# Kernel optimization log

Measured on AMD Instinct MI355X. Metric: run time of the kernel, lower is better.

The kernel has to match this reference:

```python
import jax, jax.numpy as jnp
import numpy as np

DIM = 768
NUM_HEADS = 12
HEAD_DIM = DIM // NUM_HEADS
GRID = 32  # H == W
EPS = 1e-6


def setup_inputs() -> dict:
    key = jax.random.key(0)
    ks = jax.random.split(key, 8)
    B, N = 8, GRID * GRID
    x = jax.random.normal(ks[0], (B, N, DIM), dtype=jnp.float32)
    policy = jax.random.randint(ks[1], (B, N, 1), 0, 2).astype(jnp.float32)
    qkv_w = jax.random.normal(ks[2], (3 * DIM, DIM), dtype=jnp.float32) * 0.02
    qkv_b = jax.random.normal(ks[3], (3 * DIM,), dtype=jnp.float32) * 0.02
    proj_w = jax.random.normal(ks[4], (DIM, DIM), dtype=jnp.float32) * 0.02
    proj_b = jax.random.normal(ks[5], (DIM,), dtype=jnp.float32) * 0.02
    rel_pos_h = jax.random.normal(ks[6], (2 * GRID - 1, HEAD_DIM), dtype=jnp.float32) * 0.02
    rel_pos_w = jax.random.normal(ks[7], (2 * GRID - 1, HEAD_DIM), dtype=jnp.float32) * 0.02
    return {"x": x, "policy": policy, "qkv_w": qkv_w, "qkv_b": qkv_b,
            "proj_w": proj_w, "proj_b": proj_b,
            "rel_pos_h": rel_pos_h, "rel_pos_w": rel_pos_w, "H": GRID, "W": GRID}


def _attention(x, policy, qkv_w, qkv_b, proj_w, proj_b, rel_pos_h, rel_pos_w, H, W):
    B, N, C = x.shape
    nh, hd = NUM_HEADS, C // NUM_HEADS
    scale = hd ** (-0.5)
    # qkv projection: [B,N,3C] -> [3, B*nh, N, hd]
    qkv = (x @ qkv_w.T + qkv_b).reshape(B, N, 3, nh, hd)
    qkv = qkv.transpose(2, 0, 3, 1, 4).reshape(3, B * nh, N, hd)
    q, k, v = qkv[0], qkv[1], qkv[2]
    attn = jnp.einsum("bqd,bkd->bqk", q * scale, k)  # [B*nh, N, N]
    # decomposed relative position bias (q_size == k_size == (H, W))
    coords = jnp.arange(H)
    Rh = rel_pos_h[coords[:, None] - coords[None, :] + (H - 1)]  # [H,H,hd]
    coords_w = jnp.arange(W)
    Rw = rel_pos_w[coords_w[:, None] - coords_w[None, :] + (W - 1)]  # [W,W,hd]
    r_q = q.reshape(B * nh, H, W, hd)
    rel_h = jnp.einsum("bhwc,hkc->bhwk", r_q, Rh)  # [B*nh,H,W,H]
    rel_w = jnp.einsum("bhwc,wkc->bhwk", r_q, Rw)  # [B*nh,H,W,W]
    attn = (attn.reshape(B * nh, H, W, H, W)
            + rel_h[:, :, :, :, None]
            + rel_w[:, :, :, None, :]).reshape(B * nh, N, N)
    # policy-masked softmax
    attn = attn.reshape(B, nh, N, N)
    ap = policy.reshape(B, 1, 1, N)
    ap = ap + (1.0 - ap) * jnp.eye(N, dtype=ap.dtype)  # always attend to self
    max_att = jnp.max(attn, axis=-1, keepdims=True)
    e = jnp.exp(attn - max_att).astype(jnp.float32) * ap.astype(jnp.float32)
    attn = ((e + EPS / N) / (jnp.sum(e, axis=-1, keepdims=True) + EPS)).astype(x.dtype)
    out = jnp.einsum("bqk,bkd->bqd", attn.reshape(B * nh, N, N), v)
    out = out.reshape(B, nh, N, hd).transpose(0, 2, 1, 3).reshape(B, N, C)
    return out @ proj_w.T + proj_b


def reference(x, policy, qkv_w, qkv_b, proj_w, proj_b, rel_pos_h, rel_pos_w, H, W):
    return _attention(x, policy, qkv_w, qkv_b, proj_w, proj_b, rel_pos_h, rel_pos_w, H, W)
```

## Files before the change

kernel.cpp:

```cpp
#include <hip/hip_runtime.h>
#include <hip/hip_bf16.h>

#define B_   8
#define N_   1024
#define C_   768
#define NH_  12
#define HD_  64
#define BH_  96
#define EPS_ 1e-6f
#define EPSN_ (1e-6f / 1024.0f)
#define SQ_  0.1803368801111244f
#define MNEG_ (-3.0e38f)

typedef __bf16 bf16;
typedef __attribute__((ext_vector_type(8))) __bf16  bf16x8;
typedef __attribute__((ext_vector_type(4))) __bf16  bf16x4;
typedef __attribute__((ext_vector_type(4))) float   floatx4;

#define MFMA16(a, b, c) __builtin_amdgcn_mfma_f32_16x16x32_bf16((a), (b), (c), 0, 0, 0)

__device__ __forceinline__ void gld16(const void* g, void* l) {
  typedef unsigned int u32;
  __builtin_amdgcn_global_load_lds(
      (const __attribute__((address_space(1))) u32*)g,
      (__attribute__((address_space(3))) u32*)l, 16, 0, 0);
}
__device__ __forceinline__ float bfu2f(unsigned int u) {
  union { unsigned int i; float f; } v; v.i = u << 16; return v.f;
}
__device__ __forceinline__ float bfhi2f(unsigned int u) {
  union { unsigned int i; float f; } v; v.i = u & 0xffff0000u; return v.f;
}
__device__ __forceinline__ unsigned short f2bfu(float f) {
  union { float f; unsigned int i; } v; v.f = f;
  return (unsigned short)((v.i + 0x7FFFu + ((v.i >> 16) & 1u)) >> 16);
}

__global__ __launch_bounds__(256) void prep_kernel(
    const float* __restrict__ x, const float* __restrict__ qkv_w,
    const float* __restrict__ proj_w, const float* __restrict__ relh,
    const float* __restrict__ relw,
    bf16* __restrict__ Xb, bf16* __restrict__ Wq, bf16* __restrict__ Wp,
    bf16* __restrict__ Rhb, bf16* __restrict__ Rwb) {
  int bid = blockIdx.x;
  if (bid < 8448) {
    const float* in; bf16* out; int i;
    if (bid < 6144)      { in = x;      out = Xb; i = bid * 256 + threadIdx.x; }
    else if (bid < 7872) { in = qkv_w;  out = Wq; i = (bid - 6144) * 256 + threadIdx.x; }
    else                 { in = proj_w; out = Wp; i = (bid - 7872) * 256 + threadIdx.x; }
    float4 v = ((const float4*)in)[i];
    bf16x4 o = {(bf16)v.x, (bf16)v.y, (bf16)v.z, (bf16)v.w};
    ((bf16x4*)out)[i] = o;
  } else {
    const float* in = (bid < 8464) ? relh : relw;
    bf16* out = (bid < 8464) ? Rhb : Rwb;
    int i = ((bid < 8464) ? (bid - 8448) : (bid - 8464)) * 256 + threadIdx.x;
    int r = i >> 6;
    out[i] = (r < 63) ? (bf16)(in[i] * 8.0f) : (bf16)0.0f;
  }
}

__global__ __launch_bounds__(256) void gemm_qkv(
    const bf16* __restrict__ X, const bf16* __restrict__ W,
    const float* __restrict__ bias,
    bf16* __restrict__ Qb, bf16* __restrict__ Kb, bf16* __restrict__ Vb) {
  __shared__ __align__(16) bf16 As[2][8192];
  __shared__ __align__(16) bf16 Bs[2][8192];
  const int tid = threadIdx.x;
  const int lane = tid & 63, quad = lane >> 4, c16 = lane & 15;
  const int wid = tid >> 6;
  const int wm = (wid >> 1) * 64, wn = (wid & 1) * 64;
  const int m0 = blockIdx.x * 128, n0 = blockIdx.y * 128;
  const bool flip = (blockIdx.y < 12);
  floatx4 acc[4][4];
#pragma unroll
  for (int i = 0; i < 4; ++i)
#pragma unroll
    for (int j = 0; j < 4; ++j) acc[i][j] = {0.f, 0.f, 0.f, 0.f};

  auto stage = [&](int k0, int buf) {
#pragma unroll
    for (int t = 0; t < 4; ++t) {
      int task = t * 256 + tid;
      int r = task >> 3, lg = (task & 7) ^ (r & 7);
      int wbase = (t * 256 + (tid & 192)) * 8;
      gld16(X + (size_t)(m0 + r) * 768 + k0 + lg * 8, &As[buf][wbase]);
      gld16(W + (size_t)(n0 + r) * 768 + k0 + lg * 8, &Bs[buf][wbase]);
    }
  };

  stage(0, 0);
  for (int it = 0; it < 12; ++it) {
    const int cur = it & 1;
    __syncthreads();
    if (it < 11) stage((it + 1) * 64, cur ^ 1);
#pragma unroll
    for (int kw = 0; kw < 2; ++kw) {
      bf16x8 af[4], bfr[4];
#pragma unroll
      for (int i = 0; i < 4; ++i) {
        int r = wm + i * 16 + c16, pg = (kw * 4 + quad) ^ (c16 & 7);
        af[i] = *(bf16x8*)&As[cur][r * 64 + pg * 8];
      }
#pragma unroll
      for (int j = 0; j < 4; ++j) {
        int r = wn + j * 16 + c16, pg = (kw * 4 + quad) ^ (c16 & 7);
        bfr[j] = *(bf16x8*)&Bs[cur][r * 64 + pg * 8];
      }
      if (flip) {
#pragma unroll
        for (int a = 0; a < 4; ++a)
#pragma unroll
          for (int b = 0; b < 4; ++b) acc[a][b] = MFMA16(bfr[a], af[b], acc[a][b]);
      } else {
#pragma unroll
        for (int i = 0; i < 4; ++i)
#pragma unroll
          for (int j = 0; j < 4; ++j) acc[i][j] = MFMA16(af[i], bfr[j], acc[i][j]);
      }
    }
  }
  if (flip) {
    const bool isQ = (blockIdx.y < 6);
    bf16* base = isQ ? Qb : Kb;
    const int off = isQ ? 0 : 768;
#pragma unroll
    for (int a = 0; a < 4; ++a) {
      int jb = n0 + wn + a * 16 + quad * 4;
      float4 b4 = *(const float4*)&bias[jb];
      int head = (jb - off) >> 6;
      int d = jb & 63;
#pragma unroll
      for (int b = 0; b < 4; ++b) {
        int tok = m0 + wm + b * 16 + c16;
        int bb = tok >> 10, n = tok & 1023;
        float v0 = acc[a][b][0] + b4.x, v1 = acc[a][b][1] + b4.y;
        float v2 = acc[a][b][2] + b4.z, v3 = acc[a][b][3] + b4.w;
        if (isQ) { v0 *= SQ_; v1 *= SQ_; v2 *= SQ_; v3 *= SQ_; }
        bf16x4 o = {(bf16)v0, (bf16)v1, (bf16)v2, (bf16)v3};
        *(bf16x4*)&base[(((size_t)bb * NH_ + head) * N_ + n) * HD_ + d] = o;
      }
    }
  } else {
#pragma unroll
    for (int jt = 0; jt < 4; ++jt) {
      int j = n0 + wn + jt * 16 + c16;
      float bj = bias[j];
      int rem = j - 1536, head = rem >> 6, d = rem & 63;
#pragma unroll
      for (int it = 0; it < 4; ++it) {
        int mbase = m0 + wm + it * 16 + quad * 4;
        int bb = mbase >> 10, n = mbase & 1023;
        bf16x4 o = {(bf16)(acc[it][jt][0] + bj), (bf16)(acc[it][jt][1] + bj),
                    (bf16)(acc[it][jt][2] + bj), (bf16)(acc[it][jt][3] + bj)};
        *(bf16x4*)&Vb[(((size_t)bb * NH_ + head) * HD_ + d) * N_ + n] = o;
      }
    }
  }
}

__global__ __launch_bounds__(256) void vsum_kernel(const bf16* __restrict__ Vb,
                                                   float* __restrict__ Vsum) {
  const int bh = blockIdx.x;
  const int d = threadIdx.x >> 2, part = threadIdx.x & 3;
  const bf16* Vg = Vb + (size_t)bh * (N_ * HD_) + d * N_ + part * 256;
  float s = 0.f;
  for (int i = 0; i < 32; ++i) {
    bf16x8 v = *(const bf16x8*)(Vg + i * 8);
#pragma unroll
    for (int e = 0; e < 8; ++e) s += (float)v[e];
  }
  __shared__ float red[64][4];
  red[d][part] = s;
  __syncthreads();
  if (part == 0) Vsum[bh * 64 + d] = red[d][0] + red[d][1] + red[d][2] + red[d][3];
}

__global__ __launch_bounds__(256, 3) void attn_mfma(
    const bf16* __restrict__ Qb, const bf16* __restrict__ Kb,
    const bf16* __restrict__ Vb, const float* __restrict__ policy,
    const bf16* __restrict__ Rh, const bf16* __restrict__ Rw,
    const float* __restrict__ Vsum, bf16* __restrict__ AO) {
  const int bh = blockIdx.x, qt = blockIdx.y;
  const int b = bh / NH_, head = bh % NH_;
  __shared__ __align__(16) bf16 Qs[4096];
  __shared__ __align__(16) bf16 Ks[2][4096];
  __shared__ __align__(16) bf16 Vt[2][4096];
  __shared__ unsigned short RHb[64][34];
  __shared__ unsigned short RWb[64][34];
  __shared__ __align__(16) float polf[1024];
  const int tid = threadIdx.x;
  const int wid = tid >> 6, lane = tid & 63, quad = lane >> 4, c16 = lane & 15;
  const int sw = c16 & 7;
  bf16* Ptw = Qs + wid * 1024;
  const floatx4 zero4 = {0.f, 0.f, 0.f, 0.f};

  const bf16* Qg = Qb + ((size_t)bh * N_ + qt * 64) * HD_;
  const bf16* Kg = Kb + (size_t)bh * (N_ * HD_);
  const bf16* Vg = Vb + (size_t)bh * (N_ * HD_);

  auto stageKV = [&](int kt2, int buf) {
#pragma unroll
    for (int t = 0; t < 2; ++t) {
      int task = t * 256 + tid;
      int r = task >> 3, lg = (task & 7) ^ (r & 7);
      int wbase = (t * 256 + (tid & 192)) * 8;
      gld16(Kg + (size_t)(kt2 * 64 + r) * 64 + lg * 8, &Ks[buf][wbase]);
      gld16(Vg + (size_t)r * N_ + kt2 * 64 + lg * 8, &Vt[buf][wbase]);
    }
  };

#pragma unroll
  for (int t = 0; t < 2; ++t) {
    int task = t * 256 + tid;
    int r = task >> 3, lg = (task & 7) ^ (r & 7);
    int wbase = (t * 256 + (tid & 192)) * 8;
    gld16(Qg + r * 64 + lg * 8, &Qs[wbase]);
    gld16(Rh + r * 64 + lg * 8, &Ks[0][wbase]);
  }
  gld16(policy + (size_t)b * N_ + tid * 4, &polf[(tid & 192) * 4]);
  __syncthreads();

  stageKV(0, 1);

  {
    float4 p4 = *(float4*)&polf[tid * 4];
    float4 m4 = make_float4((p4.x != 0.f) ? 0.f : MNEG_, (p4.y != 0.f) ? 0.f : MNEG_,
                            (p4.z != 0.f) ? 0.f : MNEG_, (p4.w != 0.f) ? 0.f : MNEG_);
    *(float4*)&polf[tid * 4] = m4;
  }

  bf16x8 aq0 = *(bf16x8*)&Qs[(wid * 16 + c16) * 64 + (quad ^ sw) * 8];
  bf16x8 aq1 = *(bf16x8*)&Qs[(wid * 16 + c16) * 64 + ((4 + quad) ^ sw) * 8];

  {
    floatx4 racc[4];
#pragma unroll
    for (int nt = 0; nt < 4; ++nt) {
      int r = nt * 16 + c16;
      bf16x8 b0 = *(bf16x8*)&Ks[0][r * 64 + (quad ^ sw) * 8];
      bf16x8 b1 = *(bf16x8*)&Ks[0][r * 64 + ((4 + quad) ^ sw) * 8];
      racc[nt] = MFMA16(aq1, b1, MFMA16(aq0, b0, zero4));
    }
#pragma unroll
    for (int nt = 0; nt < 4; ++nt)
#pragma unroll
      for (int reg = 0; reg < 4; ++reg) {
        int rloc = wid * 16 + quad * 4 + reg;
        int hh = 2 * qt + (rloc >> 5);
        int krow = hh + 31 - (nt * 16 + c16);
        if ((unsigned)krow < 32u) RHb[rloc][krow] = f2bfu(racc[nt][reg]);
      }
  }
  __syncthreads();
#pragma unroll
  for (int t = 0; t < 2; ++t) {
    int task = t * 256 + tid;
    int r = task >> 3, lg = (task & 7) ^ (r & 7);
    gld16(Rw + r * 64 + lg * 8, &Ks[0][(t * 256 + (tid & 192)) * 8]);
  }
  __syncthreads();
  {
    floatx4 racc[4];
#pragma unroll
    for (int nt = 0; nt < 4; ++nt) {
      int r = nt * 16 + c16;
      bf16x8 b0 = *(bf16x8*)&Ks[0][r * 64 + (quad ^ sw) * 8];
      bf16x8 b1 = *(bf16x8*)&Ks[0][r * 64 + ((4 + quad) ^ sw) * 8];
      racc[nt] = MFMA16(aq1, b1, MFMA16(aq0, b0, zero4));
    }
#pragma unroll
    for (int nt = 0; nt < 4; ++nt)
#pragma unroll
      for (int reg = 0; reg < 4; ++reg) {
        int rloc = wid * 16 + quad * 4 + reg;
        int kcol = (rloc & 31) + 31 - (nt * 16 + c16);
        if ((unsigned)kcol < 32u) RWb[rloc][kcol] = f2bfu(racc[nt][reg]);
      }
  }

  float rwv0[4], rwv1[4];
#pragma unroll
  for (int reg = 0; reg < 4; ++reg) {
    int rloc = wid * 16 + quad * 4 + reg;
    rwv0[reg] = bfu2f(RWb[rloc][c16]);
    rwv1[reg] = bfu2f(RWb[rloc][16 + c16]);
  }
  int ptoff[4][4];
#pragma unroll
  for (int reg = 0; reg < 4; ++reg) {
    int prow = quad * 4 + reg;
#pragma unroll
    for (int nt = 0; nt < 4; ++nt)
      ptoff[reg][nt] = prow * 64 + (c16 & 7) +
                       (((nt * 2 + (c16 >> 3)) ^ (prow & 7)) << 3);
  }

  float l_part[4] = {0.f, 0.f, 0.f, 0.f};
  floatx4 o_acc[4];
#pragma unroll
  for (int i = 0; i < 4; ++i) o_acc[i] = zero4;
  int nqr[4];
#pragma unroll
  for (int reg = 0; reg < 4; ++reg) nqr[reg] = qt * 64 + wid * 16 + quad * 4 + reg;

  for (int kt = 0; kt < 16; ++kt) {
    const int cur = (kt + 1) & 1;
    __syncthreads();
    if (kt < 15) stageKV(kt + 1, kt & 1);

    floatx4 init[4];
    float mv0 = polf[kt * 64 + c16],      mv1 = polf[kt * 64 + 16 + c16];
    float mv2 = polf[kt * 64 + 32 + c16], mv3 = polf[kt * 64 + 48 + c16];
#pragma unroll
    for (int reg = 0; reg < 4; ++reg) {
      int rloc = wid * 16 + quad * 4 + reg;
      unsigned int rhp = *(const unsigned int*)&RHb[rloc][kt * 2];
      float rh0 = bfu2f(rhp & 0xffffu), rh1 = bfhi2f(rhp);
      float m0 = mv0, m1 = mv1, m2 = mv2, m3 = mv3;
      if (kt == qt && c16 == quad * 4 + reg) {
        if (wid == 0) m0 = 0.f;
        else if (wid == 1) m1 = 0.f;
        else if (wid == 2) m2 = 0.f;
        else m3 = 0.f;
      }
      init[0][reg] = rh0 + rwv0[reg] + m0;
      init[1][reg] = rh0 + rwv1[reg] + m1;
      init[2][reg] = rh1 + rwv0[reg] + m2;
      init[3][reg] = rh1 + rwv1[reg] + m3;
    }

    floatx4 s[4];
#pragma unroll
    for (int nt = 0; nt < 4; ++nt) {
      int r = nt * 16 + c16;
      bf16x8 bk0 = *(bf16x8*)&Ks[cur][r * 64 + (quad ^ sw) * 8];
      bf16x8 bk1 = *(bf16x8*)&Ks[cur][r * 64 + ((4 + quad) ^ sw) * 8];
      s[nt] = MFMA16(aq1, bk1, MFMA16(aq0, bk0, init[nt]));
    }

#pragma unroll
    for (int reg = 0; reg < 4; ++reg) {
#pragma unroll
      for (int nt = 0; nt < 4; ++nt) {
        float e = exp2f(s[nt][reg]);
        l_part[reg] += e;
        Ptw[ptoff[reg][nt]] = (bf16)e;
      }
    }

#pragma unroll
    for (int kw2 = 0; kw2 < 2; ++kw2) {
      bf16x8 ap = *(bf16x8*)&Ptw[c16 * 64 + ((kw2 * 4 + quad) ^ sw) * 8];
#pragma unroll
      for (int dt = 0; dt < 4; ++dt) {
        int r = dt * 16 + c16;
        bf16x8 bv = *(bf16x8*)&Vt[cur][r * 64 + ((kw2 * 4 + quad) ^ sw) * 8];
        o_acc[dt] = MFMA16(ap, bv, o_acc[dt]);
      }
    }
  }

  float inv[4];
#pragma unroll
  for (int reg = 0; reg < 4; ++reg) {
    float l = l_part[reg];
#pragma unroll
    for (int d = 1; d < 16; d <<= 1) l += __shfl_xor(l, d, 64);
    inv[reg] = 1.f / (l + EPS_);
  }
#pragma unroll
  for (int dt = 0; dt < 4; ++dt) {
    int d = dt * 16 + c16;
    float vs = Vsum[bh * 64 + d];
#pragma unroll
    for (int reg = 0; reg < 4; ++reg) {
      float o = (o_acc[dt][reg] + EPSN_ * vs) * inv[reg];
      AO[((size_t)b * N_ + nqr[reg]) * C_ + head * HD_ + d] = (bf16)o;
    }
  }
}

__global__ __launch_bounds__(256) void gemm_proj(
    const bf16* __restrict__ A, const bf16* __restrict__ W,
    const float* __restrict__ bias, float* __restrict__ Out) {
  __shared__ __align__(16) bf16 As[2][8192];
  __shared__ __align__(16) bf16 Bs[2][8192];
  const int tid = threadIdx.x;
  const int lane = tid & 63, quad = lane >> 4, c16 = lane & 15;
  const int wid = tid >> 6;
  const int wm = (wid >> 1) * 64, wn = (wid & 1) * 64;
  const int m0 = blockIdx.x * 128, n0 = blockIdx.y * 128;
  floatx4 acc[4][4];
#pragma unroll
  for (int i = 0; i < 4; ++i)
#pragma unroll
    for (int j = 0; j < 4; ++j) acc[i][j] = {0.f, 0.f, 0.f, 0.f};

  auto stage = [&](int k0, int buf) {
#pragma unroll
    for (int t = 0; t < 4; ++t) {
      int task = t * 256 + tid;
      int r = task >> 3, lg = (task & 7) ^ (r & 7);
      int wbase = (t * 256 + (tid & 192)) * 8;
      gld16(A + (size_t)(m0 + r) * 768 + k0 + lg * 8, &As[buf][wbase]);
      gld16(W + (size_t)(n0 + r) * 768 + k0 + lg * 8, &Bs[buf][wbase]);
    }
  };

  stage(0, 0);
  for (int it = 0; it < 12; ++it) {
    const int cur = it & 1;
    __syncthreads();
    if (it < 11) stage((it + 1) * 64, cur ^ 1);
#pragma unroll
    for (int kw = 0; kw < 2; ++kw) {
      bf16x8 af[4], bfr[4];
#pragma unroll
      for (int i = 0; i < 4; ++i) {
        int r = wm + i * 16 + c16, pg = (kw * 4 + quad) ^ (c16 & 7);
        af[i] = *(bf16x8*)&As[cur][r * 64 + pg * 8];
      }
#pragma unroll
      for (int j = 0; j < 4; ++j) {
        int r = wn + j * 16 + c16, pg = (kw * 4 + quad) ^ (c16 & 7);
        bfr[j] = *(bf16x8*)&Bs[cur][r * 64 + pg * 8];
      }
#pragma unroll
      for (int a = 0; a < 4; ++a)
#pragma unroll
        for (int b = 0; b < 4; ++b) acc[a][b] = MFMA16(bfr[a], af[b], acc[a][b]);
    }
  }
#pragma unroll
  for (int a = 0; a < 4; ++a) {
    int jb = n0 + wn + a * 16 + quad * 4;
    float4 b4 = *(const float4*)&bias[jb];
#pragma unroll
    for (int b = 0; b < 4; ++b) {
      int m = m0 + wm + b * 16 + c16;
      float4 o = make_float4(acc[a][b][0] + b4.x, acc[a][b][1] + b4.y,
                             acc[a][b][2] + b4.z, acc[a][b][3] + b4.w);
      *(float4*)&Out[(size_t)m * 768 + jb] = o;
    }
  }
}

extern "C" void kernel_launch(void* const* d_in, const int* in_sizes, int n_in,
                              void* d_out, int out_size, void* d_ws, size_t ws_size,
                              hipStream_t stream) {
  const float* x      = (const float*)d_in[0];
  const float* policy = (const float*)d_in[1];
  const float* qkv_w  = (const float*)d_in[2];
  const float* qkv_b  = (const float*)d_in[3];
  const float* proj_w = (const float*)d_in[4];
  const float* proj_b = (const float*)d_in[5];
  const float* relh   = (const float*)d_in[6];
  const float* relw   = (const float*)d_in[7];

  char* ws = (char*)d_ws;
  bf16* Xbf   = (bf16*)(ws);
  bf16* Wqkv  = (bf16*)(ws + 12582912);
  bf16* Wproj = (bf16*)(ws + 16121856);
  bf16* Rhb   = (bf16*)(ws + 17301504);
  bf16* Rwb   = (bf16*)(ws + 17309696);
  bf16* Qb    = (bf16*)(ws + 17317888);
  bf16* Kb    = (bf16*)(ws + 29900800);
  bf16* Vb    = (bf16*)(ws + 42483712);
  bf16* AOb   = (bf16*)(ws + 55066624);
  float* Vsum = (float*)(ws + 67649536);

  prep_kernel<<<8480, 256, 0, stream>>>(x, qkv_w, proj_w, relh, relw,
                                        Xbf, Wqkv, Wproj, Rhb, Rwb);
  gemm_qkv<<<dim3(64, 18), 256, 0, stream>>>(Xbf, Wqkv, qkv_b, Qb, Kb, Vb);
  vsum_kernel<<<BH_, 256, 0, stream>>>(Vb, Vsum);
  attn_mfma<<<dim3(BH_, 16), 256, 0, stream>>>(Qb, Kb, Vb, policy, Rhb, Rwb,
                                               Vsum, AOb);
  gemm_proj<<<dim3(64, 6), 256, 0, stream>>>(AOb, Wproj, proj_b, (float*)d_out);
}
```

Baseline: 230.3 us.

## Keep attention probabilities in registers via transposed S and permuted K rows

The attention kernel now computes S transposed (K as the A operand, Q as B), and the K rows are loaded into shared memory in a permuted order so that the exp'd probabilities, once packed into bf16 pairs, line up directly as the A operand of the PV MFMA. This drops the per-tile LDS round trip for P and the Q staging buffer. The policy mask is now built as per-lane bitmasks through ballots instead of a float array in shared memory. Rh/Rw are read straight from global memory, several __syncthreads are removed, and launch bounds are raised to 4 blocks per CU. Risks are extra register pressure from the bitmasks and register-held P under the tighter occupancy bound, plus correctness of the intricate permutation.

```diff
diff --git a/kernel.cpp b/kernel.cpp
--- a/kernel.cpp
+++ b/kernel.cpp
@@ -176,23 +176,21 @@
   if (part == 0) Vsum[bh * 64 + d] = red[d][0] + red[d][1] + red[d][2] + red[d][3];
 }
 
-__global__ __launch_bounds__(256, 3) void attn_mfma(
+__global__ __launch_bounds__(256, 4) void attn_mfma(
     const bf16* __restrict__ Qb, const bf16* __restrict__ Kb,
     const bf16* __restrict__ Vb, const float* __restrict__ policy,
     const bf16* __restrict__ Rh, const bf16* __restrict__ Rw,
     const float* __restrict__ Vsum, bf16* __restrict__ AO) {
   const int bh = blockIdx.x, qt = blockIdx.y;
   const int b = bh / NH_, head = bh % NH_;
-  __shared__ __align__(16) bf16 Qs[4096];
   __shared__ __align__(16) bf16 Ks[2][4096];
   __shared__ __align__(16) bf16 Vt[2][4096];
-  __shared__ unsigned short RHb[64][34];
-  __shared__ unsigned short RWb[64][34];
-  __shared__ __align__(16) float polf[1024];
+  __shared__ unsigned int   RHb[64 * 16];
+  __shared__ unsigned short RWb[64 * 32];
   const int tid = threadIdx.x;
   const int wid = tid >> 6, lane = tid & 63, quad = lane >> 4, c16 = lane & 15;
   const int sw = c16 & 7;
-  bf16* Ptw = Qs + wid * 1024;
+  const int qloc = wid * 16 + c16;
   const floatx4 zero4 = {0.f, 0.f, 0.f, 0.f};
 
   const bf16* Qg = Qb + ((size_t)bh * N_ + qt * 64) * HD_;
@@ -203,44 +201,41 @@
 #pragma unroll
     for (int t = 0; t < 2; ++t) {
       int task = t * 256 + tid;
-      int r = task >> 3, lg = (task & 7) ^ (r & 7);
+      int p = task >> 3, g = task & 7;
+      int Tk = 32 * (p >> 5) + 4 * ((p >> 4) & 1) + 8 * ((p >> 2) & 3) + (p & 3);
       int wbase = (t * 256 + (tid & 192)) * 8;
-      gld16(Kg + (size_t)(kt2 * 64 + r) * 64 + lg * 8, &Ks[buf][wbase]);
-      gld16(Vg + (size_t)r * N_ + kt2 * 64 + lg * 8, &Vt[buf][wbase]);
+      gld16(Kg + (size_t)(kt2 * 64 + Tk) * 64 + ((g ^ (p & 7)) * 8), &Ks[buf][wbase]);
+      gld16(Vg + (size_t)p * N_ + kt2 * 64 + ((g ^ (p & 7)) * 8), &Vt[buf][wbase]);
     }
   };
 
-#pragma unroll
-  for (int t = 0; t < 2; ++t) {
-    int task = t * 256 + tid;
-    int r = task >> 3, lg = (task & 7) ^ (r & 7);
-    int wbase = (t * 256 + (tid & 192)) * 8;
-    gld16(Qg + r * 64 + lg * 8, &Qs[wbase]);
-    gld16(Rh + r * 64 + lg * 8, &Ks[0][wbase]);
-  }
-  gld16(policy + (size_t)b * N_ + tid * 4, &polf[(tid & 192) * 4]);
-  __syncthreads();
-
   stageKV(0, 1);
 
+  unsigned long long p64[4] = {0ull, 0ull, 0ull, 0ull};
   {
-    float4 p4 = *(float4*)&polf[tid * 4];
-    float4 m4 = make_float4((p4.x != 0.f) ? 0.f : MNEG_, (p4.y != 0.f) ? 0.f : MNEG_,
-                            (p4.z != 0.f) ? 0.f : MNEG_, (p4.w != 0.f) ? 0.f : MNEG_);
-    *(float4*)&polf[tid * 4] = m4;
-  }
-
-  bf16x8 aq0 = *(bf16x8*)&Qs[(wid * 16 + c16) * 64 + (quad ^ sw) * 8];
-  bf16x8 aq1 = *(bf16x8*)&Qs[(wid * 16 + c16) * 64 + ((4 + quad) ^ sw) * 8];
+    const float* Pg = policy + (size_t)b * N_;
+#pragma unroll
+    for (int kt = 0; kt < 16; ++kt) {
+      unsigned long long bal = __ballot(Pg[kt * 64 + lane] != 0.0f);
+      unsigned int w16 = (((unsigned int)bal >> (8 * quad)) & 0xFFu)
+                       | ((((unsigned int)(bal >> 32) >> (8 * quad)) & 0xFFu) << 8);
+      if (kt == qt && quad == ((qloc >> 3) & 3))
+        w16 |= 1u << (((qloc >> 5) << 3) | (qloc & 7));
+      p64[kt >> 2] |= (unsigned long long)w16 << (16 * (kt & 3));
+    }
+  }
+
+  bf16x8 qf0 = *(const bf16x8*)(Qg + qloc * 64 + quad * 8);
+  bf16x8 qf1 = *(const bf16x8*)(Qg + qloc * 64 + 32 + quad * 8);
 
   {
     floatx4 racc[4];
 #pragma unroll
     for (int nt = 0; nt < 4; ++nt) {
       int r = nt * 16 + c16;
-      bf16x8 b0 = *(bf16x8*)&Ks[0][r * 64 + (quad ^ sw) * 8];
-      bf16x8 b1 = *(bf16x8*)&Ks[0][r * 64 + ((4 + quad) ^ sw) * 8];
-      racc[nt] = MFMA16(aq1, b1, MFMA16(aq0, b0, zero4));
+      bf16x8 b0 = *(const bf16x8*)(Rh + r * 64 + quad * 8);
+      bf16x8 b1 = *(const bf16x8*)(Rh + r * 64 + 32 + quad * 8);
+      racc[nt] = MFMA16(qf1, b1, MFMA16(qf0, b0, zero4));
     }
 #pragma unroll
     for (int nt = 0; nt < 4; ++nt)
@@ -249,25 +244,18 @@
         int rloc = wid * 16 + quad * 4 + reg;
         int hh = 2 * qt + (rloc >> 5);
         int krow = hh + 31 - (nt * 16 + c16);
-        if ((unsigned)krow < 32u) RHb[rloc][krow] = f2bfu(racc[nt][reg]);
-      }
-  }
-  __syncthreads();
-#pragma unroll
-  for (int t = 0; t < 2; ++t) {
-    int task = t * 256 + tid;
-    int r = task >> 3, lg = (task & 7) ^ (r & 7);
-    gld16(Rw + r * 64 + lg * 8, &Ks[0][(t * 256 + (tid & 192)) * 8]);
-  }
-  __syncthreads();
+        if ((unsigned)krow < 32u)
+          ((unsigned short*)RHb)[rloc * 32 + krow] = f2bfu(racc[nt][reg]);
+      }
+  }
   {
     floatx4 racc[4];
 #pragma unroll
     for (int nt = 0; nt < 4; ++nt) {
       int r = nt * 16 + c16;
-      bf16x8 b0 = *(bf16x8*)&Ks[0][r * 64 + (quad ^ sw) * 8];
-      bf16x8 b1 = *(bf16x8*)&Ks[0][r * 64 + ((4 + quad) ^ sw) * 8];
-      racc[nt] = MFMA16(aq1, b1, MFMA16(aq0, b0, zero4));
+      bf16x8 b0 = *(const bf16x8*)(Rw + r * 64 + quad * 8);
+      bf16x8 b1 = *(const bf16x8*)(Rw + r * 64 + 32 + quad * 8);
+      racc[nt] = MFMA16(qf1, b1, MFMA16(qf0, b0, zero4));
     }
 #pragma unroll
     for (int nt = 0; nt < 4; ++nt)
@@ -275,108 +263,96 @@
       for (int reg = 0; reg < 4; ++reg) {
         int rloc = wid * 16 + quad * 4 + reg;
         int kcol = (rloc & 31) + 31 - (nt * 16 + c16);
-        if ((unsigned)kcol < 32u) RWb[rloc][kcol] = f2bfu(racc[nt][reg]);
-      }
-  }
-
-  float rwv0[4], rwv1[4];
-#pragma unroll
-  for (int reg = 0; reg < 4; ++reg) {
-    int rloc = wid * 16 + quad * 4 + reg;
-    rwv0[reg] = bfu2f(RWb[rloc][c16]);
-    rwv1[reg] = bfu2f(RWb[rloc][16 + c16]);
-  }
-  int ptoff[4][4];
-#pragma unroll
-  for (int reg = 0; reg < 4; ++reg) {
-    int prow = quad * 4 + reg;
-#pragma unroll
-    for (int nt = 0; nt < 4; ++nt)
-      ptoff[reg][nt] = prow * 64 + (c16 & 7) +
-                       (((nt * 2 + (c16 >> 3)) ^ (prow & 7)) << 3);
-  }
-
-  float l_part[4] = {0.f, 0.f, 0.f, 0.f};
+        if ((unsigned)kcol < 32u) RWb[rloc * 32 + kcol] = f2bfu(racc[nt][reg]);
+      }
+  }
+
+  float rwv[2][4];
+#pragma unroll
+  for (int p = 0; p < 2; ++p)
+#pragma unroll
+    for (int reg = 0; reg < 4; ++reg)
+      rwv[p][reg] = bfu2f(RWb[qloc * 32 + 8 * quad + 4 * p + reg]);
+
+  float l_lane = 0.f;
   floatx4 o_acc[4];
 #pragma unroll
   for (int i = 0; i < 4; ++i) o_acc[i] = zero4;
-  int nqr[4];
-#pragma unroll
-  for (int reg = 0; reg < 4; ++reg) nqr[reg] = qt * 64 + wid * 16 + quad * 4 + reg;
+
+  unsigned long long mm0 = p64[0], mm1 = p64[1], mm2 = p64[2], mm3 = p64[3];
 
   for (int kt = 0; kt < 16; ++kt) {
     const int cur = (kt + 1) & 1;
     __syncthreads();
     if (kt < 15) stageKV(kt + 1, kt & 1);
 
+    unsigned int w = (unsigned int)mm0 & 0xFFFFu;
+    mm0 = (mm0 >> 16) | (mm1 << 48);
+    mm1 = (mm1 >> 16) | (mm2 << 48);
+    mm2 = (mm2 >> 16) | (mm3 << 48);
+    mm3 >>= 16;
+    unsigned int rhp = RHb[qloc * 16 + kt];
+    float rh0 = bfu2f(rhp & 0xffffu), rh1 = bfhi2f(rhp);
     floatx4 init[4];
-    float mv0 = polf[kt * 64 + c16],      mv1 = polf[kt * 64 + 16 + c16];
-    float mv2 = polf[kt * 64 + 32 + c16], mv3 = polf[kt * 64 + 48 + c16];
-#pragma unroll
-    for (int reg = 0; reg < 4; ++reg) {
-      int rloc = wid * 16 + quad * 4 + reg;
-      unsigned int rhp = *(const unsigned int*)&RHb[rloc][kt * 2];
-      float rh0 = bfu2f(rhp & 0xffffu), rh1 = bfhi2f(rhp);
-      float m0 = mv0, m1 = mv1, m2 = mv2, m3 = mv3;
-      if (kt == qt && c16 == quad * 4 + reg) {
-        if (wid == 0) m0 = 0.f;
-        else if (wid == 1) m1 = 0.f;
-        else if (wid == 2) m2 = 0.f;
-        else m3 = 0.f;
-      }
-      init[0][reg] = rh0 + rwv0[reg] + m0;
-      init[1][reg] = rh0 + rwv1[reg] + m1;
-      init[2][reg] = rh1 + rwv0[reg] + m2;
-      init[3][reg] = rh1 + rwv1[reg] + m3;
+#pragma unroll
+    for (int t = 0; t < 4; ++t) {
+      float rh = (t < 2) ? rh0 : rh1;
+#pragma unroll
+      for (int reg = 0; reg < 4; ++reg) {
+        float base = rh + rwv[t & 1][reg];
+        init[t][reg] = ((w >> ((t >> 1) * 8 + (t & 1) * 4 + reg)) & 1u) ? base : MNEG_;
+      }
     }
 
     floatx4 s[4];
 #pragma unroll
-    for (int nt = 0; nt < 4; ++nt) {
-      int r = nt * 16 + c16;
-      bf16x8 bk0 = *(bf16x8*)&Ks[cur][r * 64 + (quad ^ sw) * 8];
-      bf16x8 bk1 = *(bf16x8*)&Ks[cur][r * 64 + ((4 + quad) ^ sw) * 8];
-      s[nt] = MFMA16(aq1, bk1, MFMA16(aq0, bk0, init[nt]));
-    }
-
-#pragma unroll
-    for (int reg = 0; reg < 4; ++reg) {
-#pragma unroll
-      for (int nt = 0; nt < 4; ++nt) {
-        float e = exp2f(s[nt][reg]);
-        l_part[reg] += e;
-        Ptw[ptoff[reg][nt]] = (bf16)e;
-      }
+    for (int t = 0; t < 4; ++t) {
+      int r = t * 16 + c16;
+      bf16x8 ak0 = *(bf16x8*)&Ks[cur][r * 64 + (quad ^ sw) * 8];
+      bf16x8 ak1 = *(bf16x8*)&Ks[cur][r * 64 + ((4 + quad) ^ sw) * 8];
+      s[t] = MFMA16(ak1, qf1, MFMA16(ak0, qf0, init[t]));
+    }
+
+    unsigned int pk[4][2];
+#pragma unroll
+    for (int t = 0; t < 4; ++t) {
+      float e0 = exp2f(s[t][0]), e1 = exp2f(s[t][1]);
+      float e2 = exp2f(s[t][2]), e3 = exp2f(s[t][3]);
+      l_lane += (e0 + e1) + (e2 + e3);
+      asm("v_cvt_pk_bf16_f32 %0, %1, %2" : "=v"(pk[t][0]) : "v"(e0), "v"(e1));
+      asm("v_cvt_pk_bf16_f32 %0, %1, %2" : "=v"(pk[t][1]) : "v"(e2), "v"(e3));
     }
 
 #pragma unroll
     for (int kw2 = 0; kw2 < 2; ++kw2) {
-      bf16x8 ap = *(bf16x8*)&Ptw[c16 * 64 + ((kw2 * 4 + quad) ^ sw) * 8];
+      union { unsigned int u[4]; bf16x8 v; } ap;
+      ap.u[0] = pk[2 * kw2][0];     ap.u[1] = pk[2 * kw2][1];
+      ap.u[2] = pk[2 * kw2 + 1][0]; ap.u[3] = pk[2 * kw2 + 1][1];
 #pragma unroll
       for (int dt = 0; dt < 4; ++dt) {
         int r = dt * 16 + c16;
         bf16x8 bv = *(bf16x8*)&Vt[cur][r * 64 + ((kw2 * 4 + quad) ^ sw) * 8];
-        o_acc[dt] = MFMA16(ap, bv, o_acc[dt]);
-      }
-    }
-  }
-
+        o_acc[dt] = MFMA16(ap.v, bv, o_acc[dt]);
+      }
+    }
+  }
+
+  l_lane += __shfl_xor(l_lane, 16, 64);
+  l_lane += __shfl_xor(l_lane, 32, 64);
   float inv[4];
 #pragma unroll
-  for (int reg = 0; reg < 4; ++reg) {
-    float l = l_part[reg];
-#pragma unroll
-    for (int d = 1; d < 16; d <<= 1) l += __shfl_xor(l, d, 64);
-    inv[reg] = 1.f / (l + EPS_);
-  }
+  for (int reg = 0; reg < 4; ++reg)
+    inv[reg] = 1.f / (__shfl(l_lane, (lane & 48) + quad * 4 + reg, 64) + EPS_);
+
 #pragma unroll
   for (int dt = 0; dt < 4; ++dt) {
     int d = dt * 16 + c16;
     float vs = Vsum[bh * 64 + d];
 #pragma unroll
     for (int reg = 0; reg < 4; ++reg) {
+      int nq = qt * 64 + wid * 16 + quad * 4 + reg;
       float o = (o_acc[dt][reg] + EPSN_ * vs) * inv[reg];
-      AO[((size_t)b * N_ + nqr[reg]) * C_ + head * HD_ + d] = (bf16)o;
+      AO[((size_t)b * N_ + nq) * C_ + head * HD_ + d] = (bf16)o;
     }
   }
 }
```

Result: no change. 232.8 us (+1.1%).
